# Optimization experiments

Hardware: AMD Instinct MI355X
Metric: run time of the kernel (lower is better)

## Reference

```python
import jax, jax.numpy as jnp
import numpy as np

N = 10000      # nodes
E = 320000     # edges (avg degree 32)
SI, VI = 256, 32   # node scalar / vector channels
SE, VE = 64, 4     # edge scalar / vector channels
SO, VO = 256, 32   # output channels
IN_S = 2 * SI + SE         # 576 (self_message=True)
IN_V = 2 * VI + VE         # 68
H = max(IN_V, VO)          # 68, GBP hidden vector dim
EPS = 1e-8


def setup_inputs() -> dict:
    key = jax.random.key(0)
    ks = jax.random.split(key, 9)
    node_s = jax.random.normal(ks[0], (N, SI), jnp.float32)
    node_v = jax.random.normal(ks[1], (N, VI, 3), jnp.float32)
    edge_s = jax.random.normal(ks[2], (E, SE), jnp.float32)
    edge_v = jax.random.normal(ks[3], (E, VE, 3), jnp.float32)
    # GBP params (stored as [in, out] so y = x @ W)
    wh = jax.random.normal(ks[4], (IN_V, H), jnp.float32) / np.sqrt(IN_V)
    ws_w = jax.random.normal(ks[5], (IN_S + H, SO), jnp.float32) / np.sqrt(IN_S + H)
    ws_b = jnp.zeros((SO,), jnp.float32)
    wv = jax.random.normal(ks[6], (H, VO), jnp.float32) / np.sqrt(H)
    edge_index = jax.random.randint(ks[7], (2, E), 0, N, jnp.int64)
    return {"node_s": node_s, "node_v": node_v, "edge_s": edge_s,
            "edge_v": edge_v, "wh": wh, "ws_w": ws_w, "ws_b": ws_b,
            "wv": wv, "edge_index": edge_index}


def reference(node_s, node_v, edge_s, edge_v, wh, ws_w, ws_b, wv, edge_index):
    n = node_s.shape[0]
    src, dst = edge_index[0], edge_index[1]
    # gather + tuple_cat((s_j, v_j), edge_attr, (s_i, v_i))
    s_cat = jnp.concatenate([node_s[src], edge_s, node_s[dst]], axis=-1)   # [E, IN_S]
    v_cat = jnp.concatenate([node_v[src], edge_v, node_v[dst]], axis=-2)   # [E, IN_V, 3]
    # GBP message (activations=(None,None), no vector gate)
    v_pre = jnp.swapaxes(v_cat, -1, -2)                # [E, 3, IN_V]
    vh = v_pre @ wh                                    # [E, 3, H]
    vn = jnp.sqrt(jnp.maximum(jnp.sum(vh * vh, axis=-2), EPS))  # _norm_no_nan, [E, H]
    s_msg = jnp.concatenate([s_cat, vn], axis=-1) @ ws_w + ws_b  # [E, SO]
    v_msg = jnp.swapaxes(vh @ wv, -1, -2)              # [E, VO, 3]
    # scatter-mean to target nodes
    agg_s = jax.ops.segment_sum(s_msg, dst, num_segments=n)       # [N, SO]
    agg_v = jax.ops.segment_sum(v_msg, dst, num_segments=n)       # [N, VO, 3]
    cnt = jax.ops.segment_sum(jnp.ones((s_msg.shape[0],), s_msg.dtype), dst,
                              num_segments=n)
    cnt = jnp.maximum(cnt, 1.0)
    out_s = agg_s / cnt[:, None]
    out_v = agg_v / cnt[:, None, None]
    # _merge(s, V): flatten vector channels and append to scalars
    return jnp.concatenate([out_s, out_v.reshape(n, 3 * VO)], axis=-1)  # [N, SO+3*VO]
```

## Files before the change

kernel.cpp:

```cpp
#include <hip/hip_runtime.h>
#include <hip/hip_bf16.h>

#define N_NODES 10000
#define E_TOT   320000

typedef __attribute__((ext_vector_type(8))) short short8;
typedef __attribute__((ext_vector_type(4))) short s16x4;
typedef __attribute__((ext_vector_type(4))) float f32x4;

#define HIST_OFF    0u
#define FILL_OFF    40000u
#define ZERO_BYTES  80000u
#define ROWPTR_OFF  80000u
#define PERM_OFF    120064u
#define PSRC_OFF    1400064u
#define PQ_OFF      2680064u
#define QV_OFF      12280064u
#define WHV4_OFF    14200064u
#define WBIG_OFF    14200576u
#define NSBF_OFF    14544640u
#define ANSB_OFF    19664640u
#define EAB_OFF     24784640u
#define AP_OFF      27984640u
#define AEV_OFF     36144640u
#define AGGV_OFF    36624640u
#define FLAGS_OFF   40464640u
#define NODES_OFF   120064u

union BfS { __hip_bfloat16 h; short s; };
__device__ __forceinline__ short f2bf(float x) { BfS u; u.h = __float2bfloat16(x); return u.s; }
__device__ __forceinline__ float bf(short x) { BfS u; u.s = x; return __bfloat162float(u.h); }
__device__ __forceinline__ float ldin(const void* p, int f32m, long i) {
  return f32m ? ((const float*)p)[i] : __bfloat162float(((const __hip_bfloat16*)p)[i]);
}
__device__ __forceinline__ int get_ei(const void* p, int i64m, long i) {
  return i64m ? (int)(((const long long*)p)[i]) : ((const int*)p)[i];
}

__global__ __launch_bounds__(256) void detect_kernel(
    const unsigned short* __restrict__ ns_u16,
    const int* __restrict__ ei_i32, int* __restrict__ flags)
{
  __shared__ int cf, ci;
  if (threadIdx.x == 0) { cf = 0; ci = 0; }
  __syncthreads();
  int c1 = 0;
  for (int i = threadIdx.x; i < 8192; i += 256) {
    unsigned e = (ns_u16[2 * i] >> 7) & 0xFF;
    if (e < 100 || e > 140) c1++;
  }
  int c2 = 0;
  for (int i = threadIdx.x; i < 4096; i += 256)
    if (ei_i32[2 * i + 1] != 0) c2++;
  atomicAdd(&cf, c1); atomicAdd(&ci, c2);
  __syncthreads();
  if (threadIdx.x == 0) {
    flags[0] = (cf > 512) ? 1 : 0;
    flags[1] = (ci < 100) ? 1 : 0;
  }
}

__global__ __launch_bounds__(256) void hist_kernel(
    const void* __restrict__ edge_index, const int* __restrict__ flags,
    int* __restrict__ hist)
{
  const int i64m = flags[1];
  int e = blockIdx.x * 256 + threadIdx.x;
  int dst = get_ei(edge_index, i64m, (long)E_TOT + e);
  atomicAdd(&hist[dst], 1);
}

__global__ __launch_bounds__(256) void scan_kernel(
    const int* __restrict__ hist, int* __restrict__ rowptr)
{
  __shared__ int part[256];
  int tid = threadIdx.x;
  int base = tid * 40;
  int s = 0;
  for (int i = 0; i < 40; ++i) { int idx = base + i; if (idx < N_NODES) s += hist[idx]; }
  part[tid] = s;
  __syncthreads();
  for (int off = 1; off < 256; off <<= 1) {
    int v = (tid >= off) ? part[tid - off] : 0;
    __syncthreads();
    part[tid] += v;
    __syncthreads();
  }
  int run = (tid > 0) ? part[tid - 1] : 0;
  for (int i = 0; i < 40; ++i) {
    int idx = base + i;
    if (idx < N_NODES) { rowptr[idx] = run; run += hist[idx]; }
  }
  if (tid == 255) rowptr[N_NODES] = run;
}

__global__ __launch_bounds__(256) void permute_kernel(
    const void* __restrict__ edge_index, const int* __restrict__ flags,
    const int* __restrict__ rowptr, int* __restrict__ fill,
    int* __restrict__ perm, int* __restrict__ psrc)
{
  const int i64m = flags[1];
  int e = blockIdx.x * 256 + threadIdx.x;
  int dst = get_ei(edge_index, i64m, (long)E_TOT + e);
  int src = get_ei(edge_index, i64m, e);
  int pos = rowptr[dst] + atomicAdd(&fill[dst], 1);
  perm[pos] = e; psrc[pos] = src;
}

__global__ __launch_bounds__(256) void prep_kernel(
    const void* __restrict__ ws_w, const void* __restrict__ wh,
    const void* __restrict__ wv, const int* __restrict__ flags,
    short* __restrict__ Wbig, float* __restrict__ whv4)
{
  const int f32m = flags[0];
  int b = blockIdx.x, tid = threadIdx.x;
  if (b < 672) {
    int flat = b * 256 + tid;
    int o = flat / 672, k = flat % 672;
    short v = 0;
    if (k < 320)      v = f2bf(ldin(ws_w, f32m, (long)k * 256 + o));
    else if (k < 388) v = f2bf(ldin(ws_w, f32m, (long)(576 + k - 320) * 256 + o));
    else if (k >= 416) v = f2bf(ldin(ws_w, f32m, (long)(k - 96) * 256 + o));
    Wbig[flat] = v;
  } else if (tid < 128) {
    int q = tid / 32, c = tid % 32;
    float acc = 0.f;
    for (int h = 0; h < 68; ++h)
      acc += ldin(wh, f32m, (32 + q) * 68 + h) * ldin(wv, f32m, h * 32 + c);
    whv4[tid] = acc;
  }
}

__global__ __launch_bounds__(256) void nsconv_kernel(
    const void* __restrict__ node_s, const int* __restrict__ flags,
    short* __restrict__ ns_bf)
{
  const int f32m = flags[0];
  int i = blockIdx.x * 256 + threadIdx.x;
  ns_bf[i] = f2bf(ldin(node_s, f32m, i));
}

__global__ __launch_bounds__(256) void node_pre(
    const void* __restrict__ node_v, const void* __restrict__ wh,
    const void* __restrict__ wv, const int* __restrict__ flags,
    short* __restrict__ PQ, short* __restrict__ QV)
{
  const int f32m = flags[0];
  int n0 = blockIdx.x * 4, tid = threadIdx.x;
  __shared__ float nv[4][96];
  __shared__ float pq[4][408];
  for (int i = tid; i < 4 * 96; i += 256) nv[i / 96][i % 96] = ldin(node_v, f32m, (long)n0 * 96 + i);
  __syncthreads();
  for (int o = tid; o < 4 * 408; o += 256) {
    int i = o / 408, r0 = o % 408;
    int part = r0 / 204, r = r0 % 204, d = r / 68, h = r % 68;
    int cbase = part ? 36 : 0;
    float acc = 0.f;
#pragma unroll
    for (int c = 0; c < 32; ++c)
      acc += nv[i][c * 3 + d] * ldin(wh, f32m, (cbase + c) * 68 + h);
    pq[i][r0] = acc;
  }
  __syncthreads();
  for (int o = tid; o < 4 * 480; o += 256) {
    int i = o / 480, k = o % 480;
    short v = 0;
    if (k < 272) {
      int h = k >> 2, d = k & 3;
      if (d < 3) v = f2bf(pq[i][d * 68 + h]);
    } else if (k < 476) {
      v = f2bf(pq[i][204 + (k - 272)]);
    }
    PQ[(long)(n0 + i) * 480 + k] = v;
  }
  for (int o = tid; o < 4 * 96; o += 256) {
    int i = o / 96, r = o % 96, d = r / 32, c = r % 32;
    float acc = 0.f;
    for (int h = 0; h < 68; ++h)
      acc += pq[i][204 + d * 68 + h] * ldin(wv, f32m, h * 32 + c);
    QV[(long)(n0 + i) * 96 + r] = f2bf(acc);
  }
}

template <int F32M>
__device__ __forceinline__ void edge_body(
    const void* __restrict__ edge_v, const void* __restrict__ edge_s,
    const void* __restrict__ wh,
    const int* __restrict__ rowptr, const int* __restrict__ perm,
    const int* __restrict__ psrc, const short* __restrict__ PQ,
    const short* __restrict__ nsb,
    short* __restrict__ ANSb, short* __restrict__ EAb,
    float* __restrict__ AP, float* __restrict__ AEV)
{
  const int lane = threadIdx.x & 63;
  const int n = blockIdx.x * 4 + (threadIdx.x >> 6);
  const int beg = rowptr[n], deg = rowptr[n + 1] - beg;
  const bool has2 = (lane < 4);
  const int h2 = 64 + lane;
  const float w4a0 = ldin(wh, F32M, 32 * 68 + lane);
  const float w4a1 = ldin(wh, F32M, 33 * 68 + lane);
  const float w4a2 = ldin(wh, F32M, 34 * 68 + lane);
  const float w4a3 = ldin(wh, F32M, 35 * 68 + lane);
  const float w4b0 = has2 ? ldin(wh, F32M, 32 * 68 + h2) : 0.f;
  const float w4b1 = has2 ? ldin(wh, F32M, 33 * 68 + h2) : 0.f;
  const float w4b2 = has2 ? ldin(wh, F32M, 34 * 68 + h2) : 0.f;
  const float w4b3 = has2 ? ldin(wh, F32M, 35 * 68 + h2) : 0.f;
  const short* pqQ = PQ + (long)n * 480 + 272;
  const float qa0 = bf(pqQ[0 * 68 + lane]);
  const float qa1 = bf(pqQ[1 * 68 + lane]);
  const float qa2 = bf(pqQ[2 * 68 + lane]);
  const float qb0 = has2 ? bf(pqQ[0 * 68 + h2]) : 0.f;
  const float qb1 = has2 ? bf(pqQ[1 * 68 + h2]) : 0.f;
  const float qb2 = has2 ? bf(pqQ[2 * 68 + h2]) : 0.f;
  float an0 = 0.f, an1 = 0.f, an2 = 0.f, an3 = 0.f;
  float ap0 = 0.f, ap1 = 0.f, ap2 = 0.f;
  float bq0 = 0.f, bq1 = 0.f, bq2 = 0.f;
  float avna = 0.f, avnb = 0.f, aes = 0.f, aev = 0.f;
  for (int e = 0; e < deg; ++e) {
    const int sv  = psrc[beg + e];
    const int eid = perm[beg + e];
    float ev0, ev1, ev2, ev3, ev4, ev5, ev6, ev7, ev8, ev9, evA, evB;
    if (F32M) {
      const float* evp = (const float*)edge_v + (long)eid * 12;
      f32x4 a = *(const f32x4*)evp;
      f32x4 b = *(const f32x4*)(evp + 4);
      f32x4 c = *(const f32x4*)(evp + 8);
      ev0 = a.x; ev1 = a.y; ev2 = a.z; ev3 = a.w;
      ev4 = b.x; ev5 = b.y; ev6 = b.z; ev7 = b.w;
      ev8 = c.x; ev9 = c.y; evA = c.z; evB = c.w;
    } else {
      const short* evp = (const short*)edge_v + (long)eid * 12;
      s16x4 a = *(const s16x4*)evp;
      s16x4 b = *(const s16x4*)(evp + 4);
      s16x4 c = *(const s16x4*)(evp + 8);
      ev0 = bf(a.x); ev1 = bf(a.y); ev2 = bf(a.z); ev3 = bf(a.w);
      ev4 = bf(b.x); ev5 = bf(b.y); ev6 = bf(b.z); ev7 = bf(b.w);
      ev8 = bf(c.x); ev9 = bf(c.y); evA = bf(c.z); evB = bf(c.w);
    }
    const short* ps = PQ + (long)sv * 480;
    s16x4 pv = *(const s16x4*)(ps + lane * 4);
    const float pa0 = bf(pv.x), pa1 = bf(pv.y), pa2 = bf(pv.z);
    s16x4 nvv = *(const s16x4*)(nsb + (long)sv * 256 + lane * 4);
    an0 += bf(nvv.x); an1 += bf(nvv.y); an2 += bf(nvv.z); an3 += bf(nvv.w);
    aes += ldin(edge_s, F32M, (long)eid * 64 + lane);
    if (lane < 12) aev += ldin(edge_v, F32M, (long)eid * 12 + lane);
    float v0 = pa0 + qa0 + ev0 * w4a0 + ev3 * w4a1 + ev6 * w4a2 + ev9 * w4a3;
    float v1 = pa1 + qa1 + ev1 * w4a0 + ev4 * w4a1 + ev7 * w4a2 + evA * w4a3;
    float v2 = pa2 + qa2 + ev2 * w4a0 + ev5 * w4a1 + ev8 * w4a2 + evB * w4a3;
    avna += sqrtf(fmaxf(v0 * v0 + v1 * v1 + v2 * v2, 1e-8f));
    ap0 += pa0; ap1 += pa1; ap2 += pa2;
    if (has2) {
      s16x4 p2 = *(const s16x4*)(ps + h2 * 4);
      const float pb0 = bf(p2.x), pb1 = bf(p2.y), pb2 = bf(p2.z);
      float u0 = pb0 + qb0 + ev0 * w4b0 + ev3 * w4b1 + ev6 * w4b2 + ev9 * w4b3;
      float u1 = pb1 + qb1 + ev1 * w4b0 + ev4 * w4b1 + ev7 * w4b2 + evA * w4b3;
      float u2 = pb2 + qb2 + ev2 * w4b0 + ev5 * w4b1 + ev8 * w4b2 + evB * w4b3;
      avnb += sqrtf(fmaxf(u0 * u0 + u1 * u1 + u2 * u2, 1e-8f));
      bq0 += pb0; bq1 += pb1; bq2 += pb2;
    }
  }
  const float inv = 1.f / fmaxf((float)deg, 1.f);
  s16x4 av;
  av.x = f2bf(an0 * inv); av.y = f2bf(an1 * inv);
  av.z = f2bf(an2 * inv); av.w = f2bf(an3 * inv);
  *(s16x4*)(ANSb + (long)n * 256 + lane * 4) = av;
  EAb[(long)n * 160 + lane] = f2bf(aes * inv);
  EAb[(long)n * 160 + 64 + lane] = f2bf(avna * inv);
  if (has2) EAb[(long)n * 160 + 128 + lane] = f2bf(avnb * inv);
  if (lane >= 4 && lane < 32) EAb[(long)n * 160 + 128 + lane] = 0;
  float* app = AP + (long)n * 204 + lane * 3;
  app[0] = ap0; app[1] = ap1; app[2] = ap2;
  if (has2) {
    float* apb = AP + (long)n * 204 + h2 * 3;
    apb[0] = bq0; apb[1] = bq1; apb[2] = bq2;
  }
  if (lane < 12) AEV[(long)n * 12 + lane] = aev;
}

__global__ __launch_bounds__(256) void edge_wave(
    const void* __restrict__ edge_v, const void* __restrict__ edge_s,
    const void* __restrict__ wh, const int* __restrict__ flags,
    const int* __restrict__ rowptr, const int* __restrict__ perm,
    const int* __restrict__ psrc, const short* __restrict__ PQ,
    const short* __restrict__ nsb,
    short* __restrict__ ANSb, short* __restrict__ EAb,
    float* __restrict__ AP, float* __restrict__ AEV)
{
  if (flags[0])
    edge_body<1>(edge_v, edge_s, wh, rowptr, perm, psrc, PQ, nsb,
                 ANSb, EAb, AP, AEV);
  else
    edge_body<0>(edge_v, edge_s, wh, rowptr, perm, psrc, PQ, nsb,
                 ANSb, EAb, AP, AEV);
}

__global__ __launch_bounds__(256) void node_gemm(
    const short* __restrict__ ANSb, const short* __restrict__ EAb,
    const short* __restrict__ nsb, const short* __restrict__ Wbig,
    float* __restrict__ NodeS)
{
  __shared__ __align__(16) short Xs[64 * 40];
  __shared__ __align__(16) short Ws[256 * 40];
  const int tid = threadIdx.x;
  const int n0 = blockIdx.x * 64;
  const int lane = tid & 63, wave = tid >> 6;
  const int frow = lane & 15, fk = (lane >> 4) * 8, q = lane >> 4;
  f32x4 acc[4][4];
#pragma unroll
  for (int ri = 0; ri < 4; ++ri)
#pragma unroll
    for (int ci = 0; ci < 4; ++ci)
      acc[ri][ci] = (f32x4){0.f, 0.f, 0.f, 0.f};
  const int se = tid >> 2, sq = tid & 3;
  const int rn = min(n0 + se, N_NODES - 1);
  for (int s = 0; s < 21; ++s) {
    short8 xv;
    if (s < 8)       xv = *(const short8*)&ANSb[(long)rn * 256 + s * 32 + sq * 8];
    else if (s < 13) xv = *(const short8*)&EAb[(long)rn * 160 + (s - 8) * 32 + sq * 8];
    else             xv = *(const short8*)&nsb[(long)rn * 256 + (s - 13) * 32 + sq * 8];
    *(short8*)&Xs[se * 40 + sq * 8] = xv;
#pragma unroll
    for (int it = 0; it < 4; ++it) {
      int flat = it * 256 + tid;
      int nn = flat >> 2, qq = flat & 3;
      *(short8*)&Ws[nn * 40 + qq * 8] = *(const short8*)&Wbig[nn * 672 + s * 32 + qq * 8];
    }
    __syncthreads();
    short8 a[4];
#pragma unroll
    for (int ri = 0; ri < 4; ++ri)
      a[ri] = *(const short8*)&Xs[(ri * 16 + frow) * 40 + fk];
#pragma unroll
    for (int ci = 0; ci < 4; ++ci) {
      int nn = wave * 64 + ci * 16 + frow;
      short8 b = *(const short8*)&Ws[nn * 40 + fk];
#pragma unroll
      for (int ri = 0; ri < 4; ++ri)
        acc[ri][ci] = __builtin_amdgcn_mfma_f32_16x16x32_bf16(a[ri], b, acc[ri][ci], 0, 0, 0);
    }
    __syncthreads();
  }
#pragma unroll
  for (int ri = 0; ri < 4; ++ri)
#pragma unroll
    for (int rr = 0; rr < 4; ++rr) {
      int row = n0 + ri * 16 + q * 4 + rr;
      if (row < N_NODES) {
#pragma unroll
        for (int ci = 0; ci < 4; ++ci) {
          int col = wave * 64 + ci * 16 + (lane & 15);
          NodeS[(long)row * 256 + col] = acc[ri][ci][rr];
        }
      }
    }
}

__global__ __launch_bounds__(256) void nodev_kernel(
    const float* __restrict__ AP, const float* __restrict__ AEV,
    const void* __restrict__ wv, const float* __restrict__ whv4,
    const int* __restrict__ flags, float* __restrict__ agg_v)
{
  const int f32m = flags[0];
  int n0 = blockIdx.x * 4, tid = threadIdx.x;
  __shared__ float wvs[68 * 32];
  __shared__ float wh4s[128];
  __shared__ float APs[4][204];
  __shared__ float AEVs[4][12];
  for (int i = tid; i < 2176; i += 256) wvs[i] = ldin(wv, f32m, i);
  if (tid < 128) wh4s[tid] = whv4[tid];
  for (int i = tid; i < 816; i += 256) APs[i / 204][i % 204] = AP[(long)n0 * 204 + i];
  if (tid < 48) AEVs[tid / 12][tid % 12] = AEV[(long)n0 * 12 + tid];
  __syncthreads();
  for (int o = tid; o < 384; o += 256) {
    int i = o / 96, r = o % 96, c = r / 3, d = r % 3;
    float acc = AEVs[i][d] * wh4s[c] + AEVs[i][3 + d] * wh4s[32 + c]
              + AEVs[i][6 + d] * wh4s[64 + c] + AEVs[i][9 + d] * wh4s[96 + c];
    for (int h = 0; h < 68; ++h)
      acc += APs[i][h * 3 + d] * wvs[h * 32 + c];
    agg_v[(long)(n0 + i) * 96 + r] = acc;
  }
}

__global__ __launch_bounds__(256) void finalize(
    const float* __restrict__ NodeS, const float* __restrict__ agg_v,
    const int* __restrict__ rowptr, const short* __restrict__ QV,
    const void* __restrict__ ws_b, const int* __restrict__ flags,
    void* __restrict__ out)
{
  const int f32m = flags[0];
  int flat = blockIdx.x * 256 + threadIdx.x;
  int n = flat / 352, j = flat % 352;
  int deg = rowptr[n + 1] - rowptr[n];
  float v;
  if (j < 256) {
    v = (deg > 0) ? (NodeS[(long)n * 256 + j] + ldin(ws_b, f32m, j)) : 0.f;
  } else {
    int m = j - 256, ch = m / 3, d = m % 3;
    float inv = 1.f / fmaxf((float)deg, 1.f);
    v = agg_v[(long)n * 96 + m] * inv;
    if (deg > 0) v += bf(QV[(long)n * 96 + d * 32 + ch]);
  }
  if (f32m) ((float*)out)[flat] = v;
  else      ((__hip_bfloat16*)out)[flat] = __float2bfloat16(v);
}

extern "C" void kernel_launch(void* const* d_in, const int* in_sizes, int n_in,
                              void* d_out, int out_size, void* d_ws, size_t ws_size,
                              hipStream_t stream) {
  const void* node_s = d_in[0];
  const void* node_v = d_in[1];
  const void* edge_s = d_in[2];
  const void* edge_v = d_in[3];
  const void* wh     = d_in[4];
  const void* ws_w   = d_in[5];
  const void* ws_b   = d_in[6];
  const void* wv     = d_in[7];
  const void* edge_index = d_in[8];

  char* ws = (char*)d_ws;
  int*   hist  = (int*)(ws + HIST_OFF);
  int*   fill  = (int*)(ws + FILL_OFF);
  int*   rowptr= (int*)(ws + ROWPTR_OFF);
  int*   perm  = (int*)(ws + PERM_OFF);
  int*   psrc  = (int*)(ws + PSRC_OFF);
  short* PQ    = (short*)(ws + PQ_OFF);
  short* QV    = (short*)(ws + QV_OFF);
  float* whv4  = (float*)(ws + WHV4_OFF);
  short* Wbig  = (short*)(ws + WBIG_OFF);
  short* ns_bf = (short*)(ws + NSBF_OFF);
  short* ANSb  = (short*)(ws + ANSB_OFF);
  short* EAb   = (short*)(ws + EAB_OFF);
  float* AP    = (float*)(ws + AP_OFF);
  float* AEV   = (float*)(ws + AEV_OFF);
  float* NodeS = (float*)(ws + NODES_OFF);
  float* agg_v = (float*)(ws + AGGV_OFF);
  int*   flags = (int*)(ws + FLAGS_OFF);

  hipMemsetAsync(d_ws, 0, ZERO_BYTES, stream);
  detect_kernel<<<1, 256, 0, stream>>>((const unsigned short*)node_s,
                                       (const int*)edge_index, flags);
  hist_kernel<<<1250, 256, 0, stream>>>(edge_index, flags, hist);
  scan_kernel<<<1, 256, 0, stream>>>(hist, rowptr);
  permute_kernel<<<1250, 256, 0, stream>>>(edge_index, flags, rowptr, fill,
                                           perm, psrc);
  prep_kernel<<<673, 256, 0, stream>>>(ws_w, wh, wv, flags, Wbig, whv4);
  nsconv_kernel<<<10000, 256, 0, stream>>>(node_s, flags, ns_bf);
  node_pre<<<2500, 256, 0, stream>>>(node_v, wh, wv, flags, PQ, QV);
  edge_wave<<<2500, 256, 0, stream>>>(edge_v, edge_s, wh, flags, rowptr,
                                      perm, psrc, PQ, ns_bf,
                                      ANSb, EAb, AP, AEV);
  node_gemm<<<157, 256, 0, stream>>>(ANSb, EAb, ns_bf, Wbig, NodeS);
  nodev_kernel<<<2500, 256, 0, stream>>>(AP, AEV, wv, whv4, flags, agg_v);
  finalize<<<13750, 256, 0, stream>>>(NodeS, agg_v, rowptr, QV, ws_b,
                                      flags, d_out);
}
```

Before: 488.3 us.

## Split each node's edges across four waves and fuse small node kernels

The edge aggregation now assigns one block per destination node, with its four waves striding over that node's edges, and prefetches the next edge's indices. Partial sums are reduced through shared memory before the outputs are written. The node_s bf16 conversion is folded into node_pre, and nodev plus finalize become a single kernel that keeps agg_v in shared memory. Together these aim to cut per-wave serial loop length, launch count and intermediate global traffic. The cost is a block barrier and shared-memory reduction per node.

```diff
diff --git a/kernel.cpp b/kernel.cpp
--- a/kernel.cpp
+++ b/kernel.cpp
@@ -131,25 +131,19 @@
   }
 }
 
-__global__ __launch_bounds__(256) void nsconv_kernel(
-    const void* __restrict__ node_s, const int* __restrict__ flags,
-    short* __restrict__ ns_bf)
-{
-  const int f32m = flags[0];
-  int i = blockIdx.x * 256 + threadIdx.x;
-  ns_bf[i] = f2bf(ldin(node_s, f32m, i));
-}
-
 __global__ __launch_bounds__(256) void node_pre(
     const void* __restrict__ node_v, const void* __restrict__ wh,
-    const void* __restrict__ wv, const int* __restrict__ flags,
-    short* __restrict__ PQ, short* __restrict__ QV)
+    const void* __restrict__ wv, const void* __restrict__ node_s,
+    const int* __restrict__ flags,
+    short* __restrict__ PQ, short* __restrict__ QV, short* __restrict__ ns_bf)
 {
   const int f32m = flags[0];
   int n0 = blockIdx.x * 4, tid = threadIdx.x;
   __shared__ float nv[4][96];
   __shared__ float pq[4][408];
   for (int i = tid; i < 4 * 96; i += 256) nv[i / 96][i % 96] = ldin(node_v, f32m, (long)n0 * 96 + i);
+  for (int i = tid; i < 1024; i += 256)
+    ns_bf[(long)n0 * 256 + i] = f2bf(ldin(node_s, f32m, (long)n0 * 256 + i));
   __syncthreads();
   for (int o = tid; o < 4 * 408; o += 256) {
     int i = o / 408, r0 = o % 408;
@@ -192,8 +186,9 @@
     short* __restrict__ ANSb, short* __restrict__ EAb,
     float* __restrict__ AP, float* __restrict__ AEV)
 {
-  const int lane = threadIdx.x & 63;
-  const int n = blockIdx.x * 4 + (threadIdx.x >> 6);
+  const int tid = threadIdx.x;
+  const int lane = tid & 63, w = tid >> 6;
+  const int n = blockIdx.x;
   const int beg = rowptr[n], deg = rowptr[n + 1] - beg;
   const bool has2 = (lane < 4);
   const int h2 = 64 + lane;
@@ -216,9 +211,12 @@
   float ap0 = 0.f, ap1 = 0.f, ap2 = 0.f;
   float bq0 = 0.f, bq1 = 0.f, bq2 = 0.f;
   float avna = 0.f, avnb = 0.f, aes = 0.f, aev = 0.f;
-  for (int e = 0; e < deg; ++e) {
-    const int sv  = psrc[beg + e];
-    const int eid = perm[beg + e];
+  int e = w;
+  int sv = 0, eid = 0;
+  if (e < deg) { sv = psrc[beg + e]; eid = perm[beg + e]; }
+  while (e < deg) {
+    int en = e + 4, svn = 0, eidn = 0;
+    if (en < deg) { svn = psrc[beg + en]; eidn = perm[beg + en]; }
     float ev0, ev1, ev2, ev3, ev4, ev5, ev6, ev7, ev8, ev9, evA, evB;
     if (F32M) {
       const float* evp = (const float*)edge_v + (long)eid * 12;
@@ -258,26 +256,52 @@
       avnb += sqrtf(fmaxf(u0 * u0 + u1 * u1 + u2 * u2, 1e-8f));
       bq0 += pb0; bq1 += pb1; bq2 += pb2;
     }
-  }
+    e = en; sv = svn; eid = eidn;
+  }
+  __shared__ float ansL[4][256];
+  __shared__ float apL[4][204];
+  __shared__ float avnL[4][132];
+  __shared__ float aesL[4][64];
+  __shared__ float aevL[4][12];
+  ansL[w][lane * 4 + 0] = an0; ansL[w][lane * 4 + 1] = an1;
+  ansL[w][lane * 4 + 2] = an2; ansL[w][lane * 4 + 3] = an3;
+  apL[w][lane * 3 + 0] = ap0; apL[w][lane * 3 + 1] = ap1; apL[w][lane * 3 + 2] = ap2;
+  if (has2) {
+    apL[w][192 + lane * 3 + 0] = bq0;
+    apL[w][192 + lane * 3 + 1] = bq1;
+    apL[w][192 + lane * 3 + 2] = bq2;
+  }
+  avnL[w][lane] = avna;
+  if (has2) avnL[w][64 + lane] = avnb;
+  aesL[w][lane] = aes;
+  if (lane < 12) aevL[w][lane] = aev;
+  __syncthreads();
   const float inv = 1.f / fmaxf((float)deg, 1.f);
-  s16x4 av;
-  av.x = f2bf(an0 * inv); av.y = f2bf(an1 * inv);
-  av.z = f2bf(an2 * inv); av.w = f2bf(an3 * inv);
-  *(s16x4*)(ANSb + (long)n * 256 + lane * 4) = av;
-  EAb[(long)n * 160 + lane] = f2bf(aes * inv);
-  EAb[(long)n * 160 + 64 + lane] = f2bf(avna * inv);
-  if (has2) EAb[(long)n * 160 + 128 + lane] = f2bf(avnb * inv);
-  if (lane >= 4 && lane < 32) EAb[(long)n * 160 + 128 + lane] = 0;
-  float* app = AP + (long)n * 204 + lane * 3;
-  app[0] = ap0; app[1] = ap1; app[2] = ap2;
-  if (has2) {
-    float* apb = AP + (long)n * 204 + h2 * 3;
-    apb[0] = bq0; apb[1] = bq1; apb[2] = bq2;
-  }
-  if (lane < 12) AEV[(long)n * 12 + lane] = aev;
-}
-
-__global__ __launch_bounds__(256) void edge_wave(
+  {
+    float s = ansL[0][tid] + ansL[1][tid] + ansL[2][tid] + ansL[3][tid];
+    ANSb[(long)n * 256 + tid] = f2bf(s * inv);
+  }
+  if (tid < 204) {
+    float s = apL[0][tid] + apL[1][tid] + apL[2][tid] + apL[3][tid];
+    AP[(long)n * 204 + tid] = s;
+  } else if (tid < 216) {
+    int c = tid - 204;
+    float s = aevL[0][c] + aevL[1][c] + aevL[2][c] + aevL[3][c];
+    AEV[(long)n * 12 + c] = s;
+  }
+  if (tid < 64) {
+    float s = aesL[0][tid] + aesL[1][tid] + aesL[2][tid] + aesL[3][tid];
+    EAb[(long)n * 160 + tid] = f2bf(s * inv);
+  } else if (tid < 132) {
+    int c = tid - 64;
+    float s = avnL[0][c] + avnL[1][c] + avnL[2][c] + avnL[3][c];
+    EAb[(long)n * 160 + 64 + c] = f2bf(s * inv);
+  } else if (tid < 160) {
+    EAb[(long)n * 160 + tid] = 0;
+  }
+}
+
+__global__ __launch_bounds__(256) void edge_block(
     const void* __restrict__ edge_v, const void* __restrict__ edge_s,
     const void* __restrict__ wh, const int* __restrict__ flags,
     const int* __restrict__ rowptr, const int* __restrict__ perm,
@@ -355,10 +379,12 @@
     }
 }
 
-__global__ __launch_bounds__(256) void nodev_kernel(
-    const float* __restrict__ AP, const float* __restrict__ AEV,
-    const void* __restrict__ wv, const float* __restrict__ whv4,
-    const int* __restrict__ flags, float* __restrict__ agg_v)
+__global__ __launch_bounds__(256) void final_fuse(
+    const float* __restrict__ NodeS, const float* __restrict__ AP,
+    const float* __restrict__ AEV, const void* __restrict__ wv,
+    const float* __restrict__ whv4, const int* __restrict__ rowptr,
+    const short* __restrict__ QV, const void* __restrict__ ws_b,
+    const int* __restrict__ flags, void* __restrict__ out)
 {
   const int f32m = flags[0];
   int n0 = blockIdx.x * 4, tid = threadIdx.x;
@@ -366,6 +392,7 @@
   __shared__ float wh4s[128];
   __shared__ float APs[4][204];
   __shared__ float AEVs[4][12];
+  __shared__ float aggL[4][96];
   for (int i = tid; i < 2176; i += 256) wvs[i] = ldin(wv, f32m, i);
   if (tid < 128) wh4s[tid] = whv4[tid];
   for (int i = tid; i < 816; i += 256) APs[i / 204][i % 204] = AP[(long)n0 * 204 + i];
@@ -377,31 +404,26 @@
               + AEVs[i][6 + d] * wh4s[64 + c] + AEVs[i][9 + d] * wh4s[96 + c];
     for (int h = 0; h < 68; ++h)
       acc += APs[i][h * 3 + d] * wvs[h * 32 + c];
-    agg_v[(long)(n0 + i) * 96 + r] = acc;
-  }
-}
-
-__global__ __launch_bounds__(256) void finalize(
-    const float* __restrict__ NodeS, const float* __restrict__ agg_v,
-    const int* __restrict__ rowptr, const short* __restrict__ QV,
-    const void* __restrict__ ws_b, const int* __restrict__ flags,
-    void* __restrict__ out)
-{
-  const int f32m = flags[0];
-  int flat = blockIdx.x * 256 + threadIdx.x;
-  int n = flat / 352, j = flat % 352;
-  int deg = rowptr[n + 1] - rowptr[n];
-  float v;
-  if (j < 256) {
-    v = (deg > 0) ? (NodeS[(long)n * 256 + j] + ldin(ws_b, f32m, j)) : 0.f;
-  } else {
-    int m = j - 256, ch = m / 3, d = m % 3;
-    float inv = 1.f / fmaxf((float)deg, 1.f);
-    v = agg_v[(long)n * 96 + m] * inv;
-    if (deg > 0) v += bf(QV[(long)n * 96 + d * 32 + ch]);
-  }
-  if (f32m) ((float*)out)[flat] = v;
-  else      ((__hip_bfloat16*)out)[flat] = __float2bfloat16(v);
+    aggL[i][r] = acc;
+  }
+  __syncthreads();
+  for (int o = tid; o < 1408; o += 256) {
+    int i = o / 352, j = o % 352;
+    int n = n0 + i;
+    int deg = rowptr[n + 1] - rowptr[n];
+    float v;
+    if (j < 256) {
+      v = (deg > 0) ? (NodeS[(long)n * 256 + j] + ldin(ws_b, f32m, j)) : 0.f;
+    } else {
+      int m = j - 256, ch = m / 3, d = m % 3;
+      float inv = 1.f / fmaxf((float)deg, 1.f);
+      v = aggL[i][m] * inv;
+      if (deg > 0) v += bf(QV[(long)n * 96 + d * 32 + ch]);
+    }
+    long flat = (long)n * 352 + j;
+    if (f32m) ((float*)out)[flat] = v;
+    else      ((__hip_bfloat16*)out)[flat] = __float2bfloat16(v);
+  }
 }
 
 extern "C" void kernel_launch(void* const* d_in, const int* in_sizes, int n_in,
@@ -433,7 +455,6 @@
   float* AP    = (float*)(ws + AP_OFF);
   float* AEV   = (float*)(ws + AEV_OFF);
   float* NodeS = (float*)(ws + NODES_OFF);
-  float* agg_v = (float*)(ws + AGGV_OFF);
   int*   flags = (int*)(ws + FLAGS_OFF);
 
   hipMemsetAsync(d_ws, 0, ZERO_BYTES, stream);
@@ -444,13 +465,12 @@
   permute_kernel<<<1250, 256, 0, stream>>>(edge_index, flags, rowptr, fill,
                                            perm, psrc);
   prep_kernel<<<673, 256, 0, stream>>>(ws_w, wh, wv, flags, Wbig, whv4);
-  nsconv_kernel<<<10000, 256, 0, stream>>>(node_s, flags, ns_bf);
-  node_pre<<<2500, 256, 0, stream>>>(node_v, wh, wv, flags, PQ, QV);
-  edge_wave<<<2500, 256, 0, stream>>>(edge_v, edge_s, wh, flags, rowptr,
-                                      perm, psrc, PQ, ns_bf,
-                                      ANSb, EAb, AP, AEV);
+  node_pre<<<2500, 256, 0, stream>>>(node_v, wh, wv, node_s, flags,
+                                     PQ, QV, ns_bf);
+  edge_block<<<10000, 256, 0, stream>>>(edge_v, edge_s, wh, flags, rowptr,
+                                        perm, psrc, PQ, ns_bf,
+                                        ANSb, EAb, AP, AEV);
   node_gemm<<<157, 256, 0, stream>>>(ANSb, EAb, ns_bf, Wbig, NodeS);
-  nodev_kernel<<<2500, 256, 0, stream>>>(AP, AEV, wv, whv4, flags, agg_v);
-  finalize<<<13750, 256, 0, stream>>>(NodeS, agg_v, rowptr, QV, ws_b,
-                                      flags, d_out);
-}
+  final_fuse<<<2500, 256, 0, stream>>>(NodeS, AP, AEV, wv, whv4, rowptr,
+                                       QV, ws_b, flags, d_out);
+}
```

Result: faster. 466.2 us (-4.5%).
